# Kernel tuning notes

Hardware: AMD Instinct MI355X
Metric: run time of the kernel (lower is better)

## Reference

```python
import jax, jax.numpy as jnp
import numpy as np
from jax import lax

B, S, F, C = 64, 2048, 256, 32


def setup_inputs() -> dict:
    key = jax.random.key(0)
    ks = jax.random.split(key, 6)
    return {
        "X": jax.random.normal(ks[0], (B, S, F), dtype=jnp.float32),
        "W": jax.random.normal(ks[1], (C, F), dtype=jnp.float32) * (1.0 / np.sqrt(F)),
        "b": jax.random.normal(ks[2], (C,), dtype=jnp.float32) * 0.01,
        "transitions": jax.random.normal(ks[3], (C, C), dtype=jnp.float32) * 0.1,
        "start_transitions": jax.random.normal(ks[4], (C,), dtype=jnp.float32) * 0.1,
        "end_transitions": jax.random.normal(ks[5], (C,), dtype=jnp.float32) * 0.1,
    }


def reference(X, W, b, transitions, start_transitions, end_transitions):
    # Affine projection to emission scores: [B, S, C]
    emissions = jnp.einsum("bsf,cf->bsc", X, W) + b
    e = jnp.moveaxis(emissions, 1, 0)  # [S, B, C] for scan over time

    alpha0 = start_transitions[None, :] + e[0]  # [B, C]

    def viterbi_step(alpha, e_t):
        # scores[b, i, j] = alpha[b, i] + T[i, j] + e_t[b, j]
        scores = alpha[:, :, None] + transitions[None, :, :] + e_t[:, None, :]
        best = jnp.max(scores, axis=1)      # [B, C]
        bp = jnp.argmax(scores, axis=1)     # [B, C] backpointers
        return best, bp

    alpha_T, backptrs = lax.scan(viterbi_step, alpha0, e[1:])  # backptrs: [S-1, B, C]

    final = alpha_T + end_transitions[None, :]
    best_score = jnp.max(final, axis=-1)              # [B]
    last_tag = jnp.argmax(final, axis=-1)             # [B]

    def backtrack(tag, bp):
        prev = jnp.take_along_axis(bp, tag[:, None], axis=1)[:, 0]
        return prev, prev

    _, prev_tags = lax.scan(backtrack, last_tag, backptrs, reverse=True)  # [S-1, B]
    path = jnp.concatenate([prev_tags, last_tag[None, :]], axis=0)        # [S, B]
    return best_score, jnp.moveaxis(path, 0, 1)  # ([B], [B, S])
```

## Files before the change

### kernel.cpp

```cpp
#include <hip/hip_runtime.h>

#define BB 64
#define SS 2048
#define FF 256
#define CC 32
#define CH 64

typedef unsigned u32x2 __attribute__((ext_vector_type(2)));

__device__ __forceinline__ void plswap16(int a_in, int& x, int& y) {
#if __has_builtin(__builtin_amdgcn_permlane16_swap)
    u32x2 r = __builtin_amdgcn_permlane16_swap((unsigned)a_in, (unsigned)a_in, false, false);
    x = (int)r[0]; y = (int)r[1];
#else
    int xx = a_in, yy;
    asm volatile("v_mov_b32 %0, %1" : "=v"(yy) : "v"(a_in));
    asm volatile("v_permlane16_swap_b32 %0, %1" : "+v"(xx), "+v"(yy));
    x = xx; y = yy;
#endif
}
__device__ __forceinline__ void plswap32(int a_in, int& x, int& y) {
#if __has_builtin(__builtin_amdgcn_permlane32_swap)
    u32x2 r = __builtin_amdgcn_permlane32_swap((unsigned)a_in, (unsigned)a_in, false, false);
    x = (int)r[0]; y = (int)r[1];
#else
    int xx = a_in, yy;
    asm volatile("v_mov_b32 %0, %1" : "=v"(yy) : "v"(a_in));
    asm volatile("v_permlane32_swap_b32 %0, %1" : "+v"(xx), "+v"(yy));
    x = xx; y = yy;
#endif
}

#if __has_builtin(__builtin_amdgcn_mov_dpp)
#define ROT1(d, s, K) d = __builtin_amdgcn_mov_dpp(s, 0x120 + K, 0xF, 0xF, false)
#else
#define ROT1(d, s, K) d = __builtin_amdgcn_update_dpp(s, s, 0x120 + K, 0xF, 0xF, false)
#endif
#define ROTALL(arr, s) \
    arr[0] = s;        \
    ROT1(arr[1], s, 1);  ROT1(arr[2], s, 2);  ROT1(arr[3], s, 3);  \
    ROT1(arr[4], s, 4);  ROT1(arr[5], s, 5);  ROT1(arr[6], s, 6);  \
    ROT1(arr[7], s, 7);  ROT1(arr[8], s, 8);  ROT1(arr[9], s, 9);  \
    ROT1(arr[10], s, 10); ROT1(arr[11], s, 11); ROT1(arr[12], s, 12); \
    ROT1(arr[13], s, 13); ROT1(arr[14], s, 14); ROT1(arr[15], s, 15)

__device__ __forceinline__ float fmax3_(float a, float b, float c) { return fmaxf(fmaxf(a, b), c); }

__global__ __launch_bounds__(256) void emis_kernel(const float* __restrict__ X,
                                                   const float* __restrict__ W,
                                                   const float* __restrict__ bias,
                                                   float* __restrict__ em) {
    __shared__ __align__(16) float xs[64 * 260];
    __shared__ __align__(16) float wsh[32 * 260];
    const int tid = threadIdx.x;
    const long rowbase = (long)blockIdx.x * 64;

    const float4* Xg = (const float4*)(X + rowbase * FF);
#pragma unroll
    for (int i = 0; i < 16; ++i) {
        int idx = tid + i * 256;
        int r = idx >> 6, c4 = idx & 63;
        *(float4*)&xs[r * 260 + c4 * 4] = Xg[idx];
    }
    const float4* Wg = (const float4*)W;
#pragma unroll
    for (int i = 0; i < 8; ++i) {
        int idx = tid + i * 256;
        int r = idx >> 6, c4 = idx & 63;
        *(float4*)&wsh[r * 260 + c4 * 4] = Wg[idx];
    }
    __syncthreads();

    const int rp = tid >> 3;
    const int cg = (tid & 7) * 4;
    const int r0 = rp * 2, r1 = rp * 2 + 1;
    float acc0[4] = {0.f, 0.f, 0.f, 0.f};
    float acc1[4] = {0.f, 0.f, 0.f, 0.f};

#pragma unroll 4
    for (int k = 0; k < 256; k += 4) {
        float4 xa = *(const float4*)&xs[r0 * 260 + k];
        float4 xb = *(const float4*)&xs[r1 * 260 + k];
#pragma unroll
        for (int jj = 0; jj < 4; ++jj) {
            float4 w = *(const float4*)&wsh[(cg + jj) * 260 + k];
            acc0[jj] = fmaf(xa.x, w.x, acc0[jj]);
            acc0[jj] = fmaf(xa.y, w.y, acc0[jj]);
            acc0[jj] = fmaf(xa.z, w.z, acc0[jj]);
            acc0[jj] = fmaf(xa.w, w.w, acc0[jj]);
            acc1[jj] = fmaf(xb.x, w.x, acc1[jj]);
            acc1[jj] = fmaf(xb.y, w.y, acc1[jj]);
            acc1[jj] = fmaf(xb.z, w.z, acc1[jj]);
            acc1[jj] = fmaf(xb.w, w.w, acc1[jj]);
        }
    }
    float4 b4 = *(const float4*)&bias[cg];
    float4 o0 = make_float4(acc0[0] + b4.x, acc0[1] + b4.y, acc0[2] + b4.z, acc0[3] + b4.w);
    float4 o1 = make_float4(acc1[0] + b4.x, acc1[1] + b4.y, acc1[2] + b4.z, acc1[3] + b4.w);
    *(float4*)&em[(rowbase + r0) * CC + cg] = o0;
    *(float4*)&em[(rowbase + r1) * CC + cg] = o1;
}

#define STEP2_ASM(avar, evar)                                                       \
    do {                                                                            \
        float x_, b_, q0_, q1_, q2_, q3_, q4_, q5_, q6_, q7_,                       \
              q8_, q9_, q10_, q11_, q12_, q13_, q14_, q15_;                         \
        asm volatile(                                                               \
            "v_mov_b32 %[x], %[aa]\n\t"                                             \
            "s_nop 1\n\t"                                                           \
            "v_permlane16_swap_b32 %[x], %[aa]\n\t"                                 \
            "s_nop 0\n\t"                                                           \
            "v_cndmask_b32 %[bb], %[aa], %[x], %[m16]\n\t"                          \
            "s_nop 1\n\t"                                                           \
            "v_add_f32 %[q0], %[bb], %[t0]\n\t"                                     \
            "v_add_f32_dpp %[q1], %[bb], %[t1] row_ror:1 row_mask:0xf bank_mask:0xf\n\t"  \
            "v_add_f32_dpp %[q2], %[bb], %[t2] row_ror:2 row_mask:0xf bank_mask:0xf\n\t"  \
            "v_add_f32_dpp %[q3], %[bb], %[t3] row_ror:3 row_mask:0xf bank_mask:0xf\n\t"  \
            "v_add_f32_dpp %[q4], %[bb], %[t4] row_ror:4 row_mask:0xf bank_mask:0xf\n\t"  \
            "v_add_f32_dpp %[q5], %[bb], %[t5] row_ror:5 row_mask:0xf bank_mask:0xf\n\t"  \
            "v_add_f32_dpp %[q6], %[bb], %[t6] row_ror:6 row_mask:0xf bank_mask:0xf\n\t"  \
            "v_add_f32_dpp %[q7], %[bb], %[t7] row_ror:7 row_mask:0xf bank_mask:0xf\n\t"  \
            "v_add_f32_dpp %[q8], %[bb], %[t8] row_ror:8 row_mask:0xf bank_mask:0xf\n\t"  \
            "v_add_f32_dpp %[q9], %[bb], %[t9] row_ror:9 row_mask:0xf bank_mask:0xf\n\t"  \
            "v_add_f32_dpp %[q10], %[bb], %[t10] row_ror:10 row_mask:0xf bank_mask:0xf\n\t" \
            "v_add_f32_dpp %[q11], %[bb], %[t11] row_ror:11 row_mask:0xf bank_mask:0xf\n\t" \
            "v_add_f32_dpp %[q12], %[bb], %[t12] row_ror:12 row_mask:0xf bank_mask:0xf\n\t" \
            "v_add_f32_dpp %[q13], %[bb], %[t13] row_ror:13 row_mask:0xf bank_mask:0xf\n\t" \
            "v_add_f32_dpp %[q14], %[bb], %[t14] row_ror:14 row_mask:0xf bank_mask:0xf\n\t" \
            "v_add_f32_dpp %[q15], %[bb], %[t15] row_ror:15 row_mask:0xf bank_mask:0xf\n\t" \
            "v_max3_f32 %[q0], %[q0], %[q1], %[q2]\n\t"                             \
            "v_max3_f32 %[q3], %[q3], %[q4], %[q5]\n\t"                             \
            "v_max3_f32 %[q6], %[q6], %[q7], %[q8]\n\t"                             \
            "v_max3_f32 %[q9], %[q9], %[q10], %[q11]\n\t"                           \
            "v_max3_f32 %[q12], %[q12], %[q13], %[q14]\n\t"                         \
            "v_max3_f32 %[q0], %[q0], %[q3], %[q6]\n\t"                             \
            "v_max3_f32 %[q9], %[q9], %[q12], %[q15]\n\t"                           \
            "v_max_f32 %[q0], %[q0], %[q9]\n\t"                                     \
            "v_mov_b32 %[x], %[q0]\n\t"                                             \
            "s_nop 1\n\t"                                                           \
            "v_permlane32_swap_b32 %[x], %[q0]\n\t"                                 \
            "s_nop 0\n\t"                                                           \
            "v_max_f32 %[q0], %[q0], %[x]\n\t"                                      \
            "v_add_f32 %[aa], %[q0], %[ee]\n\t"                                     \
            : [aa] "+v"(avar), [x] "=&v"(x_), [bb] "=&v"(b_),                       \
              [q0] "=&v"(q0_), [q1] "=&v"(q1_), [q2] "=&v"(q2_), [q3] "=&v"(q3_),   \
              [q4] "=&v"(q4_), [q5] "=&v"(q5_), [q6] "=&v"(q6_), [q7] "=&v"(q7_),   \
              [q8] "=&v"(q8_), [q9] "=&v"(q9_), [q10] "=&v"(q10_),                  \
              [q11] "=&v"(q11_), [q12] "=&v"(q12_), [q13] "=&v"(q13_),              \
              [q14] "=&v"(q14_), [q15] "=&v"(q15_)                                  \
            : [ee] "v"(evar), [t0] "v"(Ti[0]), [t1] "v"(Ti[1]), [t2] "v"(Ti[2]),    \
              [t3] "v"(Ti[3]), [t4] "v"(Ti[4]), [t5] "v"(Ti[5]), [t6] "v"(Ti[6]),   \
              [t7] "v"(Ti[7]), [t8] "v"(Ti[8]), [t9] "v"(Ti[9]), [t10] "v"(Ti[10]), \
              [t11] "v"(Ti[11]), [t12] "v"(Ti[12]), [t13] "v"(Ti[13]),              \
              [t14] "v"(Ti[14]), [t15] "v"(Ti[15]),                                 \
              [m16] "s"(mask16));                                                   \
    } while (0)

__global__ __launch_bounds__(64, 1) void viterbi_fwd4(float* __restrict__ em,
                                                      const float* __restrict__ T,
                                                      const float* __restrict__ startT,
                                                      const float* __restrict__ endT,
                                                      float* __restrict__ out) {
    const int l = threadIdx.x;
    const int b = blockIdx.x;
    const int j = l & 31;
    const int h = l >> 5;

    int p0, p1;
    plswap16(j, p0, p1);
    const bool c16 = (((p0 >> 4) & 1) == h);
    const int pm = c16 ? p0 : p1;
    int mk[16];
    ROTALL(mk, pm);

    const unsigned long long mask16 = __ballot(c16);

    float Ti[16];
#pragma unroll
    for (int k = 0; k < 16; ++k) Ti[k] = T[mk[k] * CC + j];

    float* eb = em + (long)b * SS * CC;

    float eq[8];
#pragma unroll
    for (int v = 0; v < 8; ++v) eq[v] = eb[v * 32 + j];

    float a = startT[j] + eq[0];
    eb[j] = a;
    eq[0] = eb[8 * 32 + j];

    int t = 1;
    for (int g = 0; g < 254; ++g) {
#pragma unroll
        for (int u = 0; u < 8; ++u) {
            STEP2_ASM(a, eq[t & 7]);
            eb[t * 32 + j] = a;
            eq[t & 7] = eb[(t + 8) * 32 + j];
            ++t;
        }
    }
#pragma unroll
    for (int u = 0; u < 7; ++u) {
        STEP2_ASM(a, eq[t & 7]);
        eb[t * 32 + j] = a;
        eq[t & 7] = eb[(t + 8) * 32 + j];
        ++t;
    }
#pragma unroll
    for (int u = 0; u < 8; ++u) {
        STEP2_ASM(a, eq[t & 7]);
        eb[t * 32 + j] = a;
        ++t;
    }

    float v = a + endT[j];
    int idx = j;
#pragma unroll
    for (int d = 1; d <= 16; d <<= 1) {
        float ovv = __shfl_xor(v, d);
        int   oii = __shfl_xor(idx, d);
        bool c = (ovv > v) || (ovv == v && oii < idx);
        v = c ? ovv : v;
        idx = c ? oii : idx;
    }
    if (l == 0) {
        out[b] = v;
        out[BB + (long)b * SS + (SS - 1)] = (float)idx;
    }
}

__global__ __launch_bounds__(64, 4) void bp_compose(const float* __restrict__ alpha,
                                                    const float* __restrict__ T,
                                                    unsigned* __restrict__ bp,
                                                    unsigned char* __restrict__ G) {
    const int l = threadIdx.x;
    const int j = l & 31;
    const int h = l >> 5;
    const int b = blockIdx.x >> 6;
    const int k = blockIdx.x & 63;

    int p0, p1;
    plswap16(j, p0, p1);
    const bool c16 = (((p0 >> 4) & 1) == h);
    const int pm = c16 ? p0 : p1;
    int mk[16];
    ROTALL(mk, pm);
    int q0p, q1p;
    plswap32(l, q0p, q1p);
    const bool pick0 = (q0p == (l ^ 32));

    float Ti[16];
    unsigned Bk[16];
#pragma unroll
    for (int kk = 0; kk < 16; ++kk) {
        Ti[kk] = T[mk[kk] * CC + j];
        Bk[kk] = 1u << mk[kk];
    }

    const float* A = alpha + (long)b * SS * CC;
    const int u0 = k << 5;

    float aq[8];
#pragma unroll
    for (int v = 0; v < 8; ++v) aq[v] = A[(u0 + v) * CC + j];

    unsigned sr[8];
#pragma unroll
    for (int p = 0; p < 8; ++p) sr[p] = 0u;

#pragma unroll
    for (int g8 = 0; g8 < 4; ++g8) {
#pragma unroll
        for (int v = 0; v < 8; ++v) {
            const int u = g8 * 8 + v;
            float av = aq[v];
            if (g8 < 3) aq[v] = A[(u0 + (g8 + 1) * 8 + v) * CC + j];

            int x, y;
            plswap16(__float_as_int(av), x, y);
            int base = c16 ? x : y;
            int rot[16];
            ROTALL(rot, base);
            float s[16];
#pragma unroll
            for (int kk = 0; kk < 16; ++kk) s[kk] = __int_as_float(rot[kk]) + Ti[kk];

            float m0 = fmax3_(s[0], s[1], s[2]);
            float m1 = fmax3_(s[3], s[4], s[5]);
            float m2 = fmax3_(s[6], s[7], s[8]);
            float m3 = fmax3_(s[9], s[10], s[11]);
            float m4 = fmax3_(s[12], s[13], s[14]);
            float mv = fmaxf(fmax3_(m0, m1, m2), fmax3_(m3, m4, s[15]));

            int xm, ym;
            plswap32(__float_as_int(mv), xm, ym);
            float ov = __int_as_float(pick0 ? xm : ym);
            float gv = fmaxf(mv, ov);

            unsigned c0 = (s[0] == gv) ? Bk[0] : 0u,   c1 = (s[1] == gv) ? Bk[1] : 0u;
            unsigned c2 = (s[2] == gv) ? Bk[2] : 0u,   c3 = (s[3] == gv) ? Bk[3] : 0u;
            unsigned c4 = (s[4] == gv) ? Bk[4] : 0u,   c5 = (s[5] == gv) ? Bk[5] : 0u;
            unsigned c6 = (s[6] == gv) ? Bk[6] : 0u,   c7 = (s[7] == gv) ? Bk[7] : 0u;
            unsigned c8 = (s[8] == gv) ? Bk[8] : 0u,   c9 = (s[9] == gv) ? Bk[9] : 0u;
            unsigned c10 = (s[10] == gv) ? Bk[10] : 0u, c11 = (s[11] == gv) ? Bk[11] : 0u;
            unsigned c12 = (s[12] == gv) ? Bk[12] : 0u, c13 = (s[13] == gv) ? Bk[13] : 0u;
            unsigned c14 = (s[14] == gv) ? Bk[14] : 0u, c15 = (s[15] == gv) ? Bk[15] : 0u;
            unsigned msk = ((c0 | c1 | c2) | (c3 | c4 | c5)) |
                           ((c6 | c7 | c8) | (c9 | c10 | c11)) |
                           ((c12 | c13 | c14) | c15);

            int xk, yk;
            plswap32((int)msk, xk, yk);
            unsigned om = (unsigned)(pick0 ? xk : yk);
            int wi = __builtin_ctz(msk | om);

            if (u == 31 && k == CH - 1) wi = j;
            sr[u >> 2] |= (unsigned)wi << ((u & 3) * 8);
        }
    }

#pragma unroll
    for (int p = 0; p < 8; ++p)
        bp[((unsigned)(8 * k + p) * BB + b) * CC + j] = sr[p];

    int g = j;
#pragma unroll
    for (int rel = 31; rel >= 0; --rel) {
        unsigned dw = (unsigned)__builtin_amdgcn_ds_bpermute((g | (l & 32)) << 2,
                                                             (int)sr[rel >> 2]);
        g = (int)((dw >> ((rel & 3) * 8)) & 31u);
    }
    G[(b * CH + k) * 32 + j] = (unsigned char)g;
}

__global__ __launch_bounds__(64) void bt_scan(const unsigned char* __restrict__ G,
                                              const float* __restrict__ out,
                                              int* __restrict__ tagB) {
    __shared__ unsigned char Gs[32 * CH * 32];
    const int l = threadIdx.x;
    const int bbase = blockIdx.x * 32;
    const float4* Gg = (const float4*)(G + (size_t)bbase * CH * 32);
    float4* Gls = (float4*)Gs;
#pragma unroll
    for (int i = 0; i < 64; ++i) Gls[l + i * 64] = Gg[l + i * 64];
    __syncthreads();

    if (l < 32) {
        const int b = bbase + l;
        int cur = (int)out[BB + (long)b * SS + (SS - 1)];
        for (int k = CH - 1; k >= 0; --k) {
            cur = Gs[(l * CH + k) * 32 + cur];
            tagB[b * CH + k] = cur;
        }
    }
}

__global__ __launch_bounds__(64, 4) void bt_emit(const unsigned* __restrict__ bp,
                                                 const int* __restrict__ tagB,
                                                 const float* __restrict__ outR,
                                                 float* __restrict__ out) {
    const int l = threadIdx.x;
    const int b = blockIdx.x >> 6;
    const int k = blockIdx.x & 63;

    unsigned sr[8];
#pragma unroll
    for (int p = 0; p < 8; ++p) sr[p] = bp[((unsigned)(8 * k + p) * BB + b) * CC + (l & 31)];

    int start = (k == CH - 1) ? (int)outR[BB + (long)b * SS + (SS - 1)]
                              : tagB[b * CH + k + 1];
    int g = start, cap = start;
#pragma unroll
    for (int rel = 31; rel >= 0; --rel) {
        unsigned dw = (unsigned)__builtin_amdgcn_ds_bpermute((g | (l & 32)) << 2,
                                                             (int)sr[rel >> 2]);
        g = (int)((dw >> ((rel & 3) * 8)) & 31u);
        cap = (l == rel) ? g : cap;
    }
    if (l < 32) out[BB + (long)b * SS + k * 32 + l] = (float)cap;
}

extern "C" void kernel_launch(void* const* d_in, const int* in_sizes, int n_in,
                              void* d_out, int out_size, void* d_ws, size_t ws_size,
                              hipStream_t stream) {
    const float* X      = (const float*)d_in[0];
    const float* W      = (const float*)d_in[1];
    const float* bias   = (const float*)d_in[2];
    const float* T      = (const float*)d_in[3];
    const float* startT = (const float*)d_in[4];
    const float* endT   = (const float*)d_in[5];
    float* out = (float*)d_out;

    float*    em = (float*)d_ws;
    unsigned* bp = (unsigned*)((char*)d_ws + (size_t)BB * SS * CC * 4);
    unsigned char* G    = (unsigned char*)d_ws + (20u << 20);
    int*           tagB = (int*)((char*)d_ws + (20u << 20) + 131072);

    emis_kernel<<<(BB * SS) / 64, 256, 0, stream>>>(X, W, bias, em);
    viterbi_fwd4<<<BB, 64, 0, stream>>>(em, T, startT, endT, out);
    bp_compose<<<BB * CH, 64, 0, stream>>>(em, T, bp, G);
    bt_scan<<<2, 64, 0, stream>>>(G, out, tagB);
    bt_emit<<<BB * CH, 64, 0, stream>>>(bp, tagB, out, out);
}
```

Baseline: 291.1 us.

## Interleave two batch recurrences per wavefront in Viterbi forward pass

```diff
diff --git a/kernel.cpp b/kernel.cpp
--- a/kernel.cpp
+++ b/kernel.cpp
@@ -101,68 +101,111 @@
     *(float4*)&em[(rowbase + r1) * CC + cg] = o1;
 }
 
-#define STEP2_ASM(avar, evar)                                                       \
+#define STEP2X_ASM(vA_, vB_, fA_, fB_)                                              \
     do {                                                                            \
-        float x_, b_, q0_, q1_, q2_, q3_, q4_, q5_, q6_, q7_,                       \
-              q8_, q9_, q10_, q11_, q12_, q13_, q14_, q15_;                         \
+        float xA_, bA_, xB_, bB_;                                                   \
+        float qA0_, qA1_, qA2_, qA3_, qA4_, qA5_, qA6_, qA7_,                       \
+              qA8_, qA9_, qA10_, qA11_, qA12_, qA13_, qA14_, qA15_;                 \
+        float qB0_, qB1_, qB2_, qB3_, qB4_, qB5_, qB6_, qB7_,                       \
+              qB8_, qB9_, qB10_, qB11_, qB12_, qB13_, qB14_, qB15_;                 \
         asm volatile(                                                               \
-            "v_mov_b32 %[x], %[aa]\n\t"                                             \
-            "s_nop 1\n\t"                                                           \
-            "v_permlane16_swap_b32 %[x], %[aa]\n\t"                                 \
+            "v_mov_b32 %[xA], %[aA]\n\t"                                            \
+            "v_mov_b32 %[xB], %[aB]\n\t"                                            \
             "s_nop 0\n\t"                                                           \
-            "v_cndmask_b32 %[bb], %[aa], %[x], %[m16]\n\t"                          \
-            "s_nop 1\n\t"                                                           \
-            "v_add_f32 %[q0], %[bb], %[t0]\n\t"                                     \
-            "v_add_f32_dpp %[q1], %[bb], %[t1] row_ror:1 row_mask:0xf bank_mask:0xf\n\t"  \
-            "v_add_f32_dpp %[q2], %[bb], %[t2] row_ror:2 row_mask:0xf bank_mask:0xf\n\t"  \
-            "v_add_f32_dpp %[q3], %[bb], %[t3] row_ror:3 row_mask:0xf bank_mask:0xf\n\t"  \
-            "v_add_f32_dpp %[q4], %[bb], %[t4] row_ror:4 row_mask:0xf bank_mask:0xf\n\t"  \
-            "v_add_f32_dpp %[q5], %[bb], %[t5] row_ror:5 row_mask:0xf bank_mask:0xf\n\t"  \
-            "v_add_f32_dpp %[q6], %[bb], %[t6] row_ror:6 row_mask:0xf bank_mask:0xf\n\t"  \
-            "v_add_f32_dpp %[q7], %[bb], %[t7] row_ror:7 row_mask:0xf bank_mask:0xf\n\t"  \
-            "v_add_f32_dpp %[q8], %[bb], %[t8] row_ror:8 row_mask:0xf bank_mask:0xf\n\t"  \
-            "v_add_f32_dpp %[q9], %[bb], %[t9] row_ror:9 row_mask:0xf bank_mask:0xf\n\t"  \
-            "v_add_f32_dpp %[q10], %[bb], %[t10] row_ror:10 row_mask:0xf bank_mask:0xf\n\t" \
-            "v_add_f32_dpp %[q11], %[bb], %[t11] row_ror:11 row_mask:0xf bank_mask:0xf\n\t" \
-            "v_add_f32_dpp %[q12], %[bb], %[t12] row_ror:12 row_mask:0xf bank_mask:0xf\n\t" \
-            "v_add_f32_dpp %[q13], %[bb], %[t13] row_ror:13 row_mask:0xf bank_mask:0xf\n\t" \
-            "v_add_f32_dpp %[q14], %[bb], %[t14] row_ror:14 row_mask:0xf bank_mask:0xf\n\t" \
-            "v_add_f32_dpp %[q15], %[bb], %[t15] row_ror:15 row_mask:0xf bank_mask:0xf\n\t" \
-            "v_max3_f32 %[q0], %[q0], %[q1], %[q2]\n\t"                             \
-            "v_max3_f32 %[q3], %[q3], %[q4], %[q5]\n\t"                             \
-            "v_max3_f32 %[q6], %[q6], %[q7], %[q8]\n\t"                             \
-            "v_max3_f32 %[q9], %[q9], %[q10], %[q11]\n\t"                           \
-            "v_max3_f32 %[q12], %[q12], %[q13], %[q14]\n\t"                         \
-            "v_max3_f32 %[q0], %[q0], %[q3], %[q6]\n\t"                             \
-            "v_max3_f32 %[q9], %[q9], %[q12], %[q15]\n\t"                           \
-            "v_max_f32 %[q0], %[q0], %[q9]\n\t"                                     \
-            "v_mov_b32 %[x], %[q0]\n\t"                                             \
-            "s_nop 1\n\t"                                                           \
-            "v_permlane32_swap_b32 %[x], %[q0]\n\t"                                 \
+            "v_permlane16_swap_b32 %[xA], %[aA]\n\t"                                \
+            "v_permlane16_swap_b32 %[xB], %[aB]\n\t"                                \
             "s_nop 0\n\t"                                                           \
-            "v_max_f32 %[q0], %[q0], %[x]\n\t"                                      \
-            "v_add_f32 %[aa], %[q0], %[ee]\n\t"                                     \
-            : [aa] "+v"(avar), [x] "=&v"(x_), [bb] "=&v"(b_),                       \
-              [q0] "=&v"(q0_), [q1] "=&v"(q1_), [q2] "=&v"(q2_), [q3] "=&v"(q3_),   \
-              [q4] "=&v"(q4_), [q5] "=&v"(q5_), [q6] "=&v"(q6_), [q7] "=&v"(q7_),   \
-              [q8] "=&v"(q8_), [q9] "=&v"(q9_), [q10] "=&v"(q10_),                  \
-              [q11] "=&v"(q11_), [q12] "=&v"(q12_), [q13] "=&v"(q13_),              \
-              [q14] "=&v"(q14_), [q15] "=&v"(q15_)                                  \
-            : [ee] "v"(evar), [t0] "v"(Ti[0]), [t1] "v"(Ti[1]), [t2] "v"(Ti[2]),    \
-              [t3] "v"(Ti[3]), [t4] "v"(Ti[4]), [t5] "v"(Ti[5]), [t6] "v"(Ti[6]),   \
-              [t7] "v"(Ti[7]), [t8] "v"(Ti[8]), [t9] "v"(Ti[9]), [t10] "v"(Ti[10]), \
+            "v_cndmask_b32 %[bA], %[aA], %[xA], %[m16]\n\t"                         \
+            "v_cndmask_b32 %[bB], %[aB], %[xB], %[m16]\n\t"                         \
+            "v_add_f32 %[qA0], %[bA], %[t0]\n\t"                                    \
+            "v_add_f32 %[qB0], %[bB], %[t0]\n\t"                                    \
+            "v_add_f32_dpp %[qA1], %[bA], %[t1] row_ror:1 row_mask:0xf bank_mask:0xf\n\t"  \
+            "v_add_f32_dpp %[qB1], %[bB], %[t1] row_ror:1 row_mask:0xf bank_mask:0xf\n\t"  \
+            "v_add_f32_dpp %[qA2], %[bA], %[t2] row_ror:2 row_mask:0xf bank_mask:0xf\n\t"  \
+            "v_add_f32_dpp %[qB2], %[bB], %[t2] row_ror:2 row_mask:0xf bank_mask:0xf\n\t"  \
+            "v_add_f32_dpp %[qA3], %[bA], %[t3] row_ror:3 row_mask:0xf bank_mask:0xf\n\t"  \
+            "v_add_f32_dpp %[qB3], %[bB], %[t3] row_ror:3 row_mask:0xf bank_mask:0xf\n\t"  \
+            "v_add_f32_dpp %[qA4], %[bA], %[t4] row_ror:4 row_mask:0xf bank_mask:0xf\n\t"  \
+            "v_add_f32_dpp %[qB4], %[bB], %[t4] row_ror:4 row_mask:0xf bank_mask:0xf\n\t"  \
+            "v_add_f32_dpp %[qA5], %[bA], %[t5] row_ror:5 row_mask:0xf bank_mask:0xf\n\t"  \
+            "v_add_f32_dpp %[qB5], %[bB], %[t5] row_ror:5 row_mask:0xf bank_mask:0xf\n\t"  \
+            "v_add_f32_dpp %[qA6], %[bA], %[t6] row_ror:6 row_mask:0xf bank_mask:0xf\n\t"  \
+            "v_add_f32_dpp %[qB6], %[bB], %[t6] row_ror:6 row_mask:0xf bank_mask:0xf\n\t"  \
+            "v_add_f32_dpp %[qA7], %[bA], %[t7] row_ror:7 row_mask:0xf bank_mask:0xf\n\t"  \
+            "v_add_f32_dpp %[qB7], %[bB], %[t7] row_ror:7 row_mask:0xf bank_mask:0xf\n\t"  \
+            "v_add_f32_dpp %[qA8], %[bA], %[t8] row_ror:8 row_mask:0xf bank_mask:0xf\n\t"  \
+            "v_add_f32_dpp %[qB8], %[bB], %[t8] row_ror:8 row_mask:0xf bank_mask:0xf\n\t"  \
+            "v_add_f32_dpp %[qA9], %[bA], %[t9] row_ror:9 row_mask:0xf bank_mask:0xf\n\t"  \
+            "v_add_f32_dpp %[qB9], %[bB], %[t9] row_ror:9 row_mask:0xf bank_mask:0xf\n\t"  \
+            "v_add_f32_dpp %[qA10], %[bA], %[t10] row_ror:10 row_mask:0xf bank_mask:0xf\n\t" \
+            "v_add_f32_dpp %[qB10], %[bB], %[t10] row_ror:10 row_mask:0xf bank_mask:0xf\n\t" \
+            "v_add_f32_dpp %[qA11], %[bA], %[t11] row_ror:11 row_mask:0xf bank_mask:0xf\n\t" \
+            "v_add_f32_dpp %[qB11], %[bB], %[t11] row_ror:11 row_mask:0xf bank_mask:0xf\n\t" \
+            "v_add_f32_dpp %[qA12], %[bA], %[t12] row_ror:12 row_mask:0xf bank_mask:0xf\n\t" \
+            "v_add_f32_dpp %[qB12], %[bB], %[t12] row_ror:12 row_mask:0xf bank_mask:0xf\n\t" \
+            "v_add_f32_dpp %[qA13], %[bA], %[t13] row_ror:13 row_mask:0xf bank_mask:0xf\n\t" \
+            "v_add_f32_dpp %[qB13], %[bB], %[t13] row_ror:13 row_mask:0xf bank_mask:0xf\n\t" \
+            "v_add_f32_dpp %[qA14], %[bA], %[t14] row_ror:14 row_mask:0xf bank_mask:0xf\n\t" \
+            "v_add_f32_dpp %[qB14], %[bB], %[t14] row_ror:14 row_mask:0xf bank_mask:0xf\n\t" \
+            "v_add_f32_dpp %[qA15], %[bA], %[t15] row_ror:15 row_mask:0xf bank_mask:0xf\n\t" \
+            "v_add_f32_dpp %[qB15], %[bB], %[t15] row_ror:15 row_mask:0xf bank_mask:0xf\n\t" \
+            "v_max3_f32 %[qA0], %[qA0], %[qA1], %[qA2]\n\t"                         \
+            "v_max3_f32 %[qB0], %[qB0], %[qB1], %[qB2]\n\t"                         \
+            "v_max3_f32 %[qA3], %[qA3], %[qA4], %[qA5]\n\t"                         \
+            "v_max3_f32 %[qB3], %[qB3], %[qB4], %[qB5]\n\t"                         \
+            "v_max3_f32 %[qA6], %[qA6], %[qA7], %[qA8]\n\t"                         \
+            "v_max3_f32 %[qB6], %[qB6], %[qB7], %[qB8]\n\t"                         \
+            "v_max3_f32 %[qA9], %[qA9], %[qA10], %[qA11]\n\t"                       \
+            "v_max3_f32 %[qB9], %[qB9], %[qB10], %[qB11]\n\t"                       \
+            "v_max3_f32 %[qA12], %[qA12], %[qA13], %[qA14]\n\t"                     \
+            "v_max3_f32 %[qB12], %[qB12], %[qB13], %[qB14]\n\t"                     \
+            "v_max3_f32 %[qA0], %[qA0], %[qA3], %[qA6]\n\t"                         \
+            "v_max3_f32 %[qB0], %[qB0], %[qB3], %[qB6]\n\t"                         \
+            "v_max3_f32 %[qA9], %[qA9], %[qA12], %[qA15]\n\t"                       \
+            "v_max3_f32 %[qB9], %[qB9], %[qB12], %[qB15]\n\t"                       \
+            "v_max_f32 %[qA0], %[qA0], %[qA9]\n\t"                                  \
+            "v_max_f32 %[qB0], %[qB0], %[qB9]\n\t"                                  \
+            "v_mov_b32 %[xA], %[qA0]\n\t"                                           \
+            "v_mov_b32 %[xB], %[qB0]\n\t"                                           \
+            "s_nop 0\n\t"                                                           \
+            "v_permlane32_swap_b32 %[xA], %[qA0]\n\t"                               \
+            "v_permlane32_swap_b32 %[xB], %[qB0]\n\t"                               \
+            "s_nop 0\n\t"                                                           \
+            "v_max_f32 %[qA0], %[qA0], %[xA]\n\t"                                   \
+            "v_max_f32 %[qB0], %[qB0], %[xB]\n\t"                                   \
+            "v_add_f32 %[aA], %[qA0], %[eA]\n\t"                                    \
+            "v_add_f32 %[aB], %[qB0], %[eB]\n\t"                                    \
+            : [aA] "+v"(vA_), [aB] "+v"(vB_),                                       \
+              [xA] "=&v"(xA_), [xB] "=&v"(xB_), [bA] "=&v"(bA_), [bB] "=&v"(bB_),   \
+              [qA0] "=&v"(qA0_), [qA1] "=&v"(qA1_), [qA2] "=&v"(qA2_),              \
+              [qA3] "=&v"(qA3_), [qA4] "=&v"(qA4_), [qA5] "=&v"(qA5_),              \
+              [qA6] "=&v"(qA6_), [qA7] "=&v"(qA7_), [qA8] "=&v"(qA8_),              \
+              [qA9] "=&v"(qA9_), [qA10] "=&v"(qA10_), [qA11] "=&v"(qA11_),          \
+              [qA12] "=&v"(qA12_), [qA13] "=&v"(qA13_), [qA14] "=&v"(qA14_),        \
+              [qA15] "=&v"(qA15_),                                                  \
+              [qB0] "=&v"(qB0_), [qB1] "=&v"(qB1_), [qB2] "=&v"(qB2_),              \
+              [qB3] "=&v"(qB3_), [qB4] "=&v"(qB4_), [qB5] "=&v"(qB5_),              \
+              [qB6] "=&v"(qB6_), [qB7] "=&v"(qB7_), [qB8] "=&v"(qB8_),              \
+              [qB9] "=&v"(qB9_), [qB10] "=&v"(qB10_), [qB11] "=&v"(qB11_),          \
+              [qB12] "=&v"(qB12_), [qB13] "=&v"(qB13_), [qB14] "=&v"(qB14_),        \
+              [qB15] "=&v"(qB15_)                                                   \
+            : [eA] "v"(fA_), [eB] "v"(fB_),                                         \
+              [t0] "v"(Ti[0]), [t1] "v"(Ti[1]), [t2] "v"(Ti[2]), [t3] "v"(Ti[3]),   \
+              [t4] "v"(Ti[4]), [t5] "v"(Ti[5]), [t6] "v"(Ti[6]), [t7] "v"(Ti[7]),   \
+              [t8] "v"(Ti[8]), [t9] "v"(Ti[9]), [t10] "v"(Ti[10]),                  \
               [t11] "v"(Ti[11]), [t12] "v"(Ti[12]), [t13] "v"(Ti[13]),              \
               [t14] "v"(Ti[14]), [t15] "v"(Ti[15]),                                 \
               [m16] "s"(mask16));                                                   \
     } while (0)
 
-__global__ __launch_bounds__(64, 1) void viterbi_fwd4(float* __restrict__ em,
+__global__ __launch_bounds__(64, 1) void viterbi_fwd5(float* __restrict__ em,
                                                       const float* __restrict__ T,
                                                       const float* __restrict__ startT,
                                                       const float* __restrict__ endT,
                                                       float* __restrict__ out) {
     const int l = threadIdx.x;
-    const int b = blockIdx.x;
+    const int b0 = blockIdx.x * 2;
+    const int b1 = b0 + 1;
     const int j = l & 31;
     const int h = l >> 5;
 
@@ -179,57 +222,85 @@
 #pragma unroll
     for (int k = 0; k < 16; ++k) Ti[k] = T[mk[k] * CC + j];
 
-    float* eb = em + (long)b * SS * CC;
-
-    float eq[8];
-#pragma unroll
-    for (int v = 0; v < 8; ++v) eq[v] = eb[v * 32 + j];
-
-    float a = startT[j] + eq[0];
-    eb[j] = a;
-    eq[0] = eb[8 * 32 + j];
+    float* ebA = em + (long)b0 * SS * CC;
+    float* ebB = em + (long)b1 * SS * CC;
+
+    float eqA[8], eqB[8];
+#pragma unroll
+    for (int v = 0; v < 8; ++v) { eqA[v] = ebA[v * 32 + j]; eqB[v] = ebB[v * 32 + j]; }
+
+    const float stj = startT[j];
+    float aA = stj + eqA[0];
+    float aB = stj + eqB[0];
+    ebA[j] = aA;
+    ebB[j] = aB;
+    eqA[0] = ebA[8 * 32 + j];
+    eqB[0] = ebB[8 * 32 + j];
 
     int t = 1;
     for (int g = 0; g < 254; ++g) {
 #pragma unroll
         for (int u = 0; u < 8; ++u) {
-            STEP2_ASM(a, eq[t & 7]);
-            eb[t * 32 + j] = a;
-            eq[t & 7] = eb[(t + 8) * 32 + j];
+            STEP2X_ASM(aA, aB, eqA[t & 7], eqB[t & 7]);
+            ebA[t * 32 + j] = aA;
+            ebB[t * 32 + j] = aB;
+            eqA[t & 7] = ebA[(t + 8) * 32 + j];
+            eqB[t & 7] = ebB[(t + 8) * 32 + j];
             ++t;
         }
     }
 #pragma unroll
     for (int u = 0; u < 7; ++u) {
-        STEP2_ASM(a, eq[t & 7]);
-        eb[t * 32 + j] = a;
-        eq[t & 7] = eb[(t + 8) * 32 + j];
+        STEP2X_ASM(aA, aB, eqA[t & 7], eqB[t & 7]);
+        ebA[t * 32 + j] = aA;
+        ebB[t * 32 + j] = aB;
+        eqA[t & 7] = ebA[(t + 8) * 32 + j];
+        eqB[t & 7] = ebB[(t + 8) * 32 + j];
         ++t;
     }
 #pragma unroll
     for (int u = 0; u < 8; ++u) {
-        STEP2_ASM(a, eq[t & 7]);
-        eb[t * 32 + j] = a;
+        STEP2X_ASM(aA, aB, eqA[t & 7], eqB[t & 7]);
+        ebA[t * 32 + j] = aA;
+        ebB[t * 32 + j] = aB;
         ++t;
     }
 
-    float v = a + endT[j];
-    int idx = j;
-#pragma unroll
-    for (int d = 1; d <= 16; d <<= 1) {
-        float ovv = __shfl_xor(v, d);
-        int   oii = __shfl_xor(idx, d);
-        bool c = (ovv > v) || (ovv == v && oii < idx);
-        v = c ? ovv : v;
-        idx = c ? oii : idx;
-    }
-    if (l == 0) {
-        out[b] = v;
-        out[BB + (long)b * SS + (SS - 1)] = (float)idx;
-    }
-}
-
-__global__ __launch_bounds__(64, 4) void bp_compose(const float* __restrict__ alpha,
+    {
+        float v = aA + endT[j];
+        int idx = j;
+#pragma unroll
+        for (int d = 1; d <= 16; d <<= 1) {
+            float ovv = __shfl_xor(v, d);
+            int   oii = __shfl_xor(idx, d);
+            bool c = (ovv > v) || (ovv == v && oii < idx);
+            v = c ? ovv : v;
+            idx = c ? oii : idx;
+        }
+        if (l == 0) {
+            out[b0] = v;
+            out[BB + (long)b0 * SS + (SS - 1)] = (float)idx;
+        }
+    }
+    {
+        float v = aB + endT[j];
+        int idx = j;
+#pragma unroll
+        for (int d = 1; d <= 16; d <<= 1) {
+            float ovv = __shfl_xor(v, d);
+            int   oii = __shfl_xor(idx, d);
+            bool c = (ovv > v) || (ovv == v && oii < idx);
+            v = c ? ovv : v;
+            idx = c ? oii : idx;
+        }
+        if (l == 0) {
+            out[b1] = v;
+            out[BB + (long)b1 * SS + (SS - 1)] = (float)idx;
+        }
+    }
+}
+
+__global__ __launch_bounds__(64, 2) void bp_compose(const float* __restrict__ alpha,
                                                     const float* __restrict__ T,
                                                     unsigned* __restrict__ bp,
                                                     unsigned char* __restrict__ G) {
@@ -397,7 +468,7 @@
     int*           tagB = (int*)((char*)d_ws + (20u << 20) + 131072);
 
     emis_kernel<<<(BB * SS) / 64, 256, 0, stream>>>(X, W, bias, em);
-    viterbi_fwd4<<<BB, 64, 0, stream>>>(em, T, startT, endT, out);
+    viterbi_fwd5<<<BB / 2, 64, 0, stream>>>(em, T, startT, endT, out);
     bp_compose<<<BB * CH, 64, 0, stream>>>(em, T, bp, G);
     bt_scan<<<2, 64, 0, stream>>>(G, out, tagB);
     bt_emit<<<BB * CH, 64, 0, stream>>>(bp, tagB, out, out);
```

Measured after the change: 425.8 us. 1.46x slower.
